# Performance work log

Hardware: AMD Instinct MI355X
Metric: run time of the kernel (lower is better)

Reference implementation:

```python
import jax, jax.numpy as jnp
import numpy as np

# Model / data dimensions
B, N, F_ATOM, V = 256, 256, 9, 128   # graphs, nodes/graph, atom feat cols, padded vocab
EMB, HID, DEPTH = 256, 32, 3          # emb_dim, hidden_channels=32 (fixed in source), depth
RATIO = 0.5                            # pool_ratios


def setup_inputs() -> dict:
    key = jax.random.key(0)
    ks = jax.random.split(key, 10)
    p = 16.0 / N  # avg degree ~16
    u = jax.random.uniform(ks[0], (B, N, N))
    adj = (u < p).astype(jnp.float32)
    adj = jnp.maximum(adj, adj.transpose(0, 2, 1))  # symmetric
    adj = adj * (1.0 - jnp.eye(N, dtype=jnp.float32))  # no self loops
    x_atom = jax.random.randint(ks[1], (B, N, F_ATOM), 0, 119)
    s = lambda k, sh, fan: jax.random.normal(k, sh) * (1.0 / np.sqrt(fan))
    return dict(
        adj=adj,
        x_atom=x_atom,
        atom_table=jax.random.normal(ks[2], (F_ATOM, V, EMB)) * 0.02,
        w_down0=s(ks[3], (EMB, HID), EMB), b_down0=jnp.zeros((HID,)),
        w_down=s(ks[4], (DEPTH, HID, HID), HID), b_down=jnp.zeros((DEPTH, HID)),
        w_pool=jax.random.normal(ks[5], (DEPTH, HID)),
        w_up=s(ks[6], (DEPTH - 1, HID, HID), HID), b_up=jnp.zeros((DEPTH - 1, HID)),
        w_up_last=s(ks[7], (HID, EMB), HID), b_up_last=jnp.zeros((EMB,)),
    )


def _gcn(x, A, W, b):
    # GCNConv(improved=True): Ahat = A + 2I, sym-normalized; A has zero diag.
    n = A.shape[-1]
    Ah = A + 2.0 * jnp.eye(n, dtype=A.dtype)
    d = jnp.sum(Ah, axis=-1)
    di = jnp.where(d > 0, jax.lax.rsqrt(jnp.maximum(d, 1e-12)), 0.0)
    An = Ah * di[:, :, None] * di[:, None, :]
    return jnp.einsum('bij,bjd->bid', An, x @ W) + b


def _augment(A):
    # remove self loops, add self loops (w=1), A @ A (spspmm), remove self loops
    n = A.shape[-1]
    eye = jnp.eye(n, dtype=A.dtype)
    A1 = A * (1.0 - eye) + eye
    A2 = jnp.einsum('bij,bjk->bik', A1, A1)
    return A2 * (1.0 - eye)


def _topk(x, A, w):
    # TopKPooling: score = tanh(x.w / ||w||); keep top ceil(ratio*n) per graph
    score = jnp.tanh((x @ w) / jnp.linalg.norm(w))  # [B, n]
    k = int(np.ceil(RATIO * x.shape[1]))
    vals, idx = jax.lax.top_k(score, k)  # [B, k]
    xg = jnp.take_along_axis(x, idx[:, :, None], axis=1) * vals[:, :, None]
    Ar = jnp.take_along_axis(A, idx[:, :, None], axis=1)
    Ag = jnp.take_along_axis(Ar, idx[:, None, :], axis=2)
    return xg, Ag, idx


def reference(adj, x_atom, atom_table, w_down0, b_down0, w_down, b_down,
              w_pool, w_up, b_up, w_up_last, b_up_last):
    # AtomEncoder: sum of per-column embeddings -> [B, N, EMB]
    h = jnp.sum(atom_table[jnp.arange(F_ATOM), x_atom], axis=2)

    # GraphUNet encode (sum_res=True, act=relu)
    x = jax.nn.relu(_gcn(h, adj, w_down0, b_down0))
    A = adj
    xs, As, perms = [x], [A], []
    for i in range(DEPTH):
        A = _augment(A)
        x, A, idx = _topk(x, A, w_pool[i])
        x = jax.nn.relu(_gcn(x, A, w_down[i], b_down[i]))
        if i < DEPTH - 1:
            xs.append(x)
            As.append(A)
        perms.append(idx)

    for i in range(DEPTH):
        j = DEPTH - 1 - i
        res, A, idx = xs[j], As[j], perms[j]
        b_idx = jnp.arange(B)[:, None]
        up = jnp.zeros_like(res).at[b_idx, idx].set(x)
        x = res + up
        if i < DEPTH - 1:
            x = jax.nn.relu(_gcn(x, A, w_up[i], b_up[i]))
        else:
            x = _gcn(x, A, w_up_last, b_up_last)

    # global_add_pool over nodes of each graph -> [B, EMB]
    return jnp.sum(x, axis=1)
```

## Files before the change

kernel.cpp:

```cpp
#include <hip/hip_runtime.h>
#include <stdint.h>
#include <math.h>

#define NB 256
#define NN 256
#define HC 32
#define EMBD 256
#define NF 9
#define NV 128
#define TPB 1024

typedef unsigned int u32;
typedef unsigned long long u64;

__global__ void k_tw(const float* __restrict__ table, const float* __restrict__ W0,
                     float* __restrict__ TW) {
    int gid = blockIdx.x * 256 + threadIdx.x;
    if (gid >= NF * NV * HC) return;
    int c = gid & 31;
    int v = (gid >> 5) & (NV - 1);
    int f = gid >> 12;
    const float* trow = table + (size_t)(f * NV + v) * EMBD;
    float acc = 0.f;
    for (int e = 0; e < EMBD; ++e) acc += trow[e] * W0[e * HC + c];
    TW[gid] = acc;
}

#define SM_BITS   0
#define SM_DI0    8192
#define SM_BIG0   9216
#define SM_X1     46080
#define SM_BIG1   64512
#define SM_X2     82944
#define SM_BIG2   92160
#define SM_ZB     101376
#define SM_WG     119808
#define SM_SC     124416
#define SM_KEYS   125440
#define SM_IDX0   127488
#define SM_VALS0  128000
#define SM_INV0   128512
#define SM_IDX1   129536
#define SM_VALS1  129792
#define SM_INV1   130048
#define SM_IDX2   130560
#define SM_VALS2  130688
#define SM_INV2   130816
#define SM_DI1    131072
#define SM_DI2    131584
#define SM_DI3    131840
#define SM_PART   131968
#define SM_GL     136192
#define SM_TOTAL  136320

__device__ __forceinline__ u32 dot4acc(u32 a, u32 b, u32 c) {
#if __has_builtin(__builtin_amdgcn_udot4)
    return __builtin_amdgcn_udot4(a, b, c, false);
#else
    return c + (a & 0xffu) * (b & 0xffu) + ((a >> 8) & 0xffu) * ((b >> 8) & 0xffu)
         + ((a >> 16) & 0xffu) * ((b >> 16) & 0xffu) + (a >> 24) * (b >> 24);
#endif
}

template <int N, int K>
__device__ __forceinline__ void topk_rank(const float* sc, u64* keys,
                                          int* idxo, float* valso, int* invo, int t) {
    if (t < N) {
        invo[t] = -1;
        float s = sc[t];
        u32 bits = __float_as_uint(s);
        u32 m = ((int)bits < 0) ? 0xFFFFFFFFu : 0x80000000u;
        u32 ordv = ~(bits ^ m);
        keys[t] = ((u64)ordv << 32) | (u32)t;
    }
    __syncthreads();
    if (t < N) {
        u64 mykey = keys[t];
        int rank = 0;
#pragma unroll 8
        for (int j = 0; j < N; ++j) rank += (keys[j] < mykey) ? 1 : 0;
        if (rank < K) {
            idxo[rank] = t;
            valso[rank] = sc[t];
            invo[t] = rank;
        }
    }
    __syncthreads();
}

template <int N>
__device__ __forceinline__ void az_f32(const float* A, const float* z,
                                       const float* di, const float* __restrict__ bias,
                                       float* xout, int t) {
    if (t < N * 8) {
        int r = t >> 3, cq = (t & 7) * 4;
        float a0 = 0.f, a1 = 0.f, a2 = 0.f, a3 = 0.f;
        for (int jj = 0; jj < N; ++jj) {
            const float4 zv = *reinterpret_cast<const float4*>(&z[jj * 36 + cq]);
            float a = A[jj * N + r];
            a0 += a * zv.x; a1 += a * zv.y; a2 += a * zv.z; a3 += a * zv.w;
        }
        float dr = di[r];
        float4 o;
        o.x = fmaxf(dr * (a0 + 2.f * z[r * 36 + cq + 0]) + bias[cq + 0], 0.f);
        o.y = fmaxf(dr * (a1 + 2.f * z[r * 36 + cq + 1]) + bias[cq + 1], 0.f);
        o.z = fmaxf(dr * (a2 + 2.f * z[r * 36 + cq + 2]) + bias[cq + 2], 0.f);
        o.w = fmaxf(dr * (a3 + 2.f * z[r * 36 + cq + 3]) + bias[cq + 3], 0.f);
        *reinterpret_cast<float4*>(&xout[r * 36 + cq]) = o;
    }
    __syncthreads();
}

__device__ __forceinline__ void az_u8(const u32* AgW, const float* z,
                                      const float* di, const float* __restrict__ bias,
                                      float* xout, int t) {
    int r = t >> 3, cq = (t & 7) * 4;
    int wsel = r >> 2, bsh = (r & 3) * 8;
    float a0 = 0.f, a1 = 0.f, a2 = 0.f, a3 = 0.f;
    for (int jj = 0; jj < 128; ++jj) {
        const float4 zv = *reinterpret_cast<const float4*>(&z[jj * 36 + cq]);
        float f = (float)((AgW[jj * 32 + wsel] >> bsh) & 255u);
        a0 += f * zv.x; a1 += f * zv.y; a2 += f * zv.z; a3 += f * zv.w;
    }
    float dr = di[r];
    float4 o;
    o.x = fmaxf(dr * (a0 + 2.f * z[r * 36 + cq + 0]) + bias[cq + 0], 0.f);
    o.y = fmaxf(dr * (a1 + 2.f * z[r * 36 + cq + 1]) + bias[cq + 1], 0.f);
    o.z = fmaxf(dr * (a2 + 2.f * z[r * 36 + cq + 2]) + bias[cq + 2], 0.f);
    o.w = fmaxf(dr * (a3 + 2.f * z[r * 36 + cq + 3]) + bias[cq + 3], 0.f);
    *reinterpret_cast<float4*>(&xout[r * 36 + cq]) = o;
    __syncthreads();
}

template <int N>
__device__ __forceinline__ void xw_mm(const float* xin, const float* Wl,
                                      const float* pre, float* zout, int t) {
    for (int i = t; i < N * 8; i += TPB) {
        int r = i >> 3, cq = (i & 7) * 4;
        float a0 = 0.f, a1 = 0.f, a2 = 0.f, a3 = 0.f;
#pragma unroll 8
        for (int e = 0; e < 32; ++e) {
            float xv = xin[r * 36 + e];
            const float4 wv = *reinterpret_cast<const float4*>(&Wl[e * 36 + cq]);
            a0 += xv * wv.x; a1 += xv * wv.y; a2 += xv * wv.z; a3 += xv * wv.w;
        }
        float p = pre ? pre[r] : 1.f;
        *reinterpret_cast<float4*>(&zout[r * 36 + cq]) =
            make_float4(a0 * p, a1 * p, a2 * p, a3 * p);
    }
    __syncthreads();
}

template <int N>
__device__ __forceinline__ void deg_lds(const float* A, float* di, int t) {
    if (t < N) {
        float acc = 0.f;
        for (int i = 0; i < N; ++i) acc += A[i * N + t];
        di[t] = 1.0f / sqrtf(acc + 2.0f);
    }
    __syncthreads();
}

__device__ __forceinline__ void deg_u8(const u32* AgW, float* di, int t) {
    if (t < 128) {
        u32 acc = 0;
        for (int w = 0; w < 32; ++w)
            acc = dot4acc(AgW[t * 32 + ((w + t) & 31)], 0x01010101u, acc);
        di[t] = 1.0f / sqrtf((float)acc + 2.0f);
    }
    __syncthreads();
}

__device__ __forceinline__ void aug64_32(const float* A, const int* idxl,
                                         float* out, int t) {
    if (t < 256) {
        int rr0 = t >> 3, sb = (t & 7) * 4;
        int ir = idxl[rr0];
        int is0 = idxl[sb], is1 = idxl[sb + 1], is2 = idxl[sb + 2], is3 = idxl[sb + 3];
        float c0 = 0.f, c1 = 0.f, c2 = 0.f, c3 = 0.f;
        for (int jj = 0; jj < 16; ++jj) {
            int jq = ((jj + rr0) & 15) * 4;
            const float4 ar = *reinterpret_cast<const float4*>(&A[ir * 64 + jq]);
            const float4 v0 = *reinterpret_cast<const float4*>(&A[is0 * 64 + jq]);
            const float4 v1 = *reinterpret_cast<const float4*>(&A[is1 * 64 + jq]);
            const float4 v2 = *reinterpret_cast<const float4*>(&A[is2 * 64 + jq]);
            const float4 v3 = *reinterpret_cast<const float4*>(&A[is3 * 64 + jq]);
            c0 += ar.x * v0.x + ar.y * v0.y + ar.z * v0.z + ar.w * v0.w;
            c1 += ar.x * v1.x + ar.y * v1.y + ar.z * v1.z + ar.w * v1.w;
            c2 += ar.x * v2.x + ar.y * v2.y + ar.z * v2.z + ar.w * v2.w;
            c3 += ar.x * v3.x + ar.y * v3.y + ar.z * v3.z + ar.w * v3.w;
        }
        float o0 = c0 + 2.f * A[ir * 64 + is0] + (ir == is0 ? 1.f : 0.f);
        float o1 = c1 + 2.f * A[ir * 64 + is1] + (ir == is1 ? 1.f : 0.f);
        float o2 = c2 + 2.f * A[ir * 64 + is2] + (ir == is2 ? 1.f : 0.f);
        float o3 = c3 + 2.f * A[ir * 64 + is3] + (ir == is3 ? 1.f : 0.f);
        if (rr0 == sb + 0) o0 = 0.f;
        if (rr0 == sb + 1) o1 = 0.f;
        if (rr0 == sb + 2) o2 = 0.f;
        if (rr0 == sb + 3) o3 = 0.f;
        *reinterpret_cast<float4*>(&out[rr0 * 32 + sb]) = make_float4(o0, o1, o2, o3);
    }
    __syncthreads();
}

__global__ void __launch_bounds__(TPB, 1) k_mega(
    const float* __restrict__ adj, const float* __restrict__ TW,
    const int* __restrict__ xa,
    const float* __restrict__ bd0, const float* __restrict__ wd,
    const float* __restrict__ bd, const float* __restrict__ wp,
    const float* __restrict__ wu, const float* __restrict__ bu,
    const float* __restrict__ wul, const float* __restrict__ bul,
    float* __restrict__ gx0, float* __restrict__ outp) {
    __shared__ __align__(16) char SM[SM_TOTAL];
    u32*   bitsl = (u32*)(SM + SM_BITS);
    float* di0l  = (float*)(SM + SM_DI0);
    float* z0    = (float*)(SM + SM_BIG0);
    u32*   AgW   = (u32*)(SM + SM_BIG0);
    float* x1l   = (float*)(SM + SM_X1);
    float* big1  = (float*)(SM + SM_BIG1);
    float* x2l   = (float*)(SM + SM_X2);
    float* big2  = (float*)(SM + SM_BIG2);
    float* zbf   = (float*)(SM + SM_ZB);
    u32*   Pg    = (u32*)(SM + SM_WG);
    float* Wl    = (float*)(SM + SM_WG);
    float* scl   = (float*)(SM + SM_SC);
    u64*   keys  = (u64*)(SM + SM_KEYS);
    int*   idx0l = (int*)(SM + SM_IDX0);
    float* vals0l= (float*)(SM + SM_VALS0);
    int*   inv0l = (int*)(SM + SM_INV0);
    int*   idx1l = (int*)(SM + SM_IDX1);
    float* vals1l= (float*)(SM + SM_VALS1);
    int*   inv1l = (int*)(SM + SM_INV1);
    int*   idx2l = (int*)(SM + SM_IDX2);
    float* vals2l= (float*)(SM + SM_VALS2);
    int*   inv2l = (int*)(SM + SM_INV2);
    float* di1   = (float*)(SM + SM_DI1);
    float* di2   = (float*)(SM + SM_DI2);
    float* di3   = (float*)(SM + SM_DI3);
    float* part  = (float*)(SM + SM_PART);
    float* gl    = (float*)(SM + SM_GL);
    float* x3l   = big2 + 1024;
    float* dec64 = big2;
    float* dec128= big1;

    int b = blockIdx.x, t = threadIdx.x;

    for (int i = t; i < 2048; i += TPB) {
        int node = i >> 3, cq = (i & 7) * 4;
        const int* xr = xa + (b * NN + node) * NF;
        float ax = 0.f, ay = 0.f, azz = 0.f, aw = 0.f;
#pragma unroll
        for (int f = 0; f < NF; ++f) {
            int v = xr[f];
            const float4 tw = *reinterpret_cast<const float4*>(&TW[((f << 7) + v) * HC + cq]);
            ax += tw.x; ay += tw.y; azz += tw.z; aw += tw.w;
        }
        *reinterpret_cast<float4*>(&z0[node * 36 + cq]) = make_float4(ax, ay, azz, aw);
    }

    {
        int lane = t & 63, wv = t >> 6;
        for (int row = wv; row < NN; row += 16) {
            const float* ar = adj + ((size_t)b * NN + row) * NN;
            int deg = 0;
#pragma unroll
            for (int p = 0; p < 4; ++p) {
                u64 m = __ballot(ar[p * 64 + lane] != 0.0f);
                if (lane == 0) {
                    bitsl[row * 8 + 2 * p]     = (u32)m;
                    bitsl[row * 8 + 2 * p + 1] = (u32)(m >> 32);
                    deg += __popcll(m);
                }
            }
            if (lane == 0) di0l[row] = 1.0f / sqrtf((float)deg + 2.0f);
        }
    }
    if (t < 32) gl[t] = wp[t];
    __syncthreads();

    {
        float sn0 = 0.f;
        for (int i = 0; i < HC; ++i) { float v = gl[i]; sn0 += v * v; }
        sn0 = sqrtf(sn0);
        int r0 = t >> 3, cq = (t & 7) * 4;
        for (int tile = 0; tile < 2; ++tile) {
            int r = tile * 128 + r0;
            u32 mw[8];
#pragma unroll
            for (int w = 0; w < 8; ++w) mw[w] = bitsl[r * 8 + w];
            float a0 = 0.f, a1 = 0.f, a2 = 0.f, a3 = 0.f;
#pragma unroll
            for (int w = 0; w < 8; ++w) {
                u32 m = mw[w];
                int base = w * 32;
                while (m) {
                    int j = base + __ffs(m) - 1;
                    m &= m - 1;
                    float dj = di0l[j];
                    const float4 zv = *reinterpret_cast<const float4*>(&z0[j * 36 + cq]);
                    a0 += dj * zv.x; a1 += dj * zv.y; a2 += dj * zv.z; a3 += dj * zv.w;
                }
            }
            float dr = di0l[r];
            float o0 = fmaxf(dr * (a0 + 2.f * dr * z0[r * 36 + cq + 0]) + bd0[cq + 0], 0.f);
            float o1 = fmaxf(dr * (a1 + 2.f * dr * z0[r * 36 + cq + 1]) + bd0[cq + 1], 0.f);
            float o2 = fmaxf(dr * (a2 + 2.f * dr * z0[r * 36 + cq + 2]) + bd0[cq + 2], 0.f);
            float o3 = fmaxf(dr * (a3 + 2.f * dr * z0[r * 36 + cq + 3]) + bd0[cq + 3], 0.f);
            *reinterpret_cast<float4*>(&gx0[((size_t)b * NN + r) * HC + cq]) =
                make_float4(o0, o1, o2, o3);
            float pd = o0 * gl[cq] + o1 * gl[cq + 1] + o2 * gl[cq + 2] + o3 * gl[cq + 3];
            pd += __shfl_xor(pd, 1);
            pd += __shfl_xor(pd, 2);
            pd += __shfl_xor(pd, 4);
            if ((t & 7) == 0) scl[r] = tanhf(pd / sn0);
        }
    }
    __syncthreads();

    topk_rank<256, 128>(scl, keys, idx0l, vals0l, inv0l, t);

    if (t < 1024) {
        int r = t >> 3, w = t & 7;
        int row = idx0l[r];
        u32 word = bitsl[row * 8 + w];
        if (w == (row >> 5)) word |= (1u << (row & 31));
        Pg[r * 9 + w] = word;
    }
    __syncthreads();
    {
        int rr0 = t >> 4, sb = (t & 15) * 4;
        u32 rw[2][8];
#pragma unroll
        for (int rt = 0; rt < 2; ++rt)
#pragma unroll
            for (int w = 0; w < 8; ++w) rw[rt][w] = Pg[(rt * 64 + rr0) * 9 + w];
#pragma unroll
        for (int k4 = 0; k4 < 2; ++k4) {
            int s0 = sb + 64 * k4;
            u32 cnt[2][4];
#pragma unroll
            for (int a = 0; a < 2; ++a) { cnt[a][0] = cnt[a][1] = cnt[a][2] = cnt[a][3] = 0; }
#pragma unroll
            for (int u = 0; u < 4; ++u) {
                int s = s0 + u;
#pragma unroll
                for (int w = 0; w < 8; ++w) {
                    u32 sw = Pg[s * 9 + w];
                    cnt[0][u] += __popc(rw[0][w] & sw);
                    cnt[1][u] += __popc(rw[1][w] & sw);
                }
            }
#pragma unroll
            for (int rt = 0; rt < 2; ++rt) {
                int r = rt * 64 + rr0;
                if (r >= s0 && r < s0 + 4) cnt[rt][r - s0] = 0;
                AgW[r * 32 + (s0 >> 2)] =
                    cnt[rt][0] | (cnt[rt][1] << 8) | (cnt[rt][2] << 16) | (cnt[rt][3] << 24);
            }
        }
    }
    __syncthreads();

    deg_u8(AgW, di1, t);

    if (t < 1024) Wl[(t >> 5) * 36 + (t & 31)] = wd[t];
    {
        int r = t >> 3, cq = (t & 7) * 4;
        float s = di1[r] * vals0l[r];
        const float4 xv = *reinterpret_cast<const float4*>(
            &gx0[((size_t)b * NN + idx0l[r]) * HC + cq]);
        *reinterpret_cast<float4*>(&big1[r * 36 + cq]) =
            make_float4(s * xv.x, s * xv.y, s * xv.z, s * xv.w);
    }
    __syncthreads();
    xw_mm<128>(big1, Wl, nullptr, zbf, t);
    az_u8(AgW, zbf, di1, bd, x1l, t);

    if (t < 32) gl[t] = wp[32 + t];
    __syncthreads();
    {
        float sn = 0.f;
        for (int i = 0; i < HC; ++i) { float v = gl[i]; sn += v * v; }
        sn = sqrtf(sn);
        if (t < 128) {
            float acc = 0.f;
#pragma unroll
            for (int i = 0; i < HC; ++i) {
                int c = (i + t) & 31;
                acc += x1l[t * 36 + c] * gl[c];
            }
            scl[t] = tanhf(acc / sn);
        }
    }
    __syncthreads();
    topk_rank<128, 64>(scl, keys, idx1l, vals1l, inv1l, t);

    {
        u32* Gb = (u32*)zbf;
        for (int i = t; i < 2048; i += TPB) {
            int k = i >> 5, w = i & 31;
            int ir = idx1l[k];
            u32 word = AgW[ir * 32 + w];
            if (w == (ir >> 2)) word += (1u << (8 * (ir & 3)));
            Gb[k * 33 + w] = word;
        }
        __syncthreads();
        {
            int r = t >> 4, sq = t & 15;
            u32 racc[4] = {0, 0, 0, 0};
            for (int w = 0; w < 32; ++w) {
                u32 rv = Gb[r * 33 + w];
                racc[0] = dot4acc(rv, Gb[(sq * 4 + 0) * 33 + w], racc[0]);
                racc[1] = dot4acc(rv, Gb[(sq * 4 + 1) * 33 + w], racc[1]);
                racc[2] = dot4acc(rv, Gb[(sq * 4 + 2) * 33 + w], racc[2]);
                racc[3] = dot4acc(rv, Gb[(sq * 4 + 3) * 33 + w], racc[3]);
            }
            float4 o;
            o.x = (r == sq * 4 + 0) ? 0.f : (float)racc[0];
            o.y = (r == sq * 4 + 1) ? 0.f : (float)racc[1];
            o.z = (r == sq * 4 + 2) ? 0.f : (float)racc[2];
            o.w = (r == sq * 4 + 3) ? 0.f : (float)racc[3];
            *reinterpret_cast<float4*>(&big1[r * 64 + sq * 4]) = o;
        }
        __syncthreads();
    }

    deg_lds<64>(big1, di2, t);

    if (t < 1024) Wl[(t >> 5) * 36 + (t & 31)] = wd[1024 + t];
    if (t < 512) {
        float* xg1 = zbf + 2304;
        int r = t >> 3, cq = (t & 7) * 4;
        float s = di2[r] * vals1l[r];
        const float4 xv = *reinterpret_cast<const float4*>(&x1l[idx1l[r] * 36 + cq]);
        *reinterpret_cast<float4*>(&xg1[r * 36 + cq]) =
            make_float4(s * xv.x, s * xv.y, s * xv.z, s * xv.w);
    }
    __syncthreads();
    xw_mm<64>(zbf + 2304, Wl, nullptr, zbf, t);
    az_f32<64>(big1, zbf, di2, bd + 32, x2l, t);

    if (t < 32) gl[t] = wp[64 + t];
    __syncthreads();
    {
        float sn = 0.f;
        for (int i = 0; i < HC; ++i) { float v = gl[i]; sn += v * v; }
        sn = sqrtf(sn);
        if (t < 64) {
            float acc = 0.f;
#pragma unroll
            for (int i = 0; i < HC; ++i) {
                int c = (i + t) & 31;
                acc += x2l[t * 36 + c] * gl[c];
            }
            scl[t] = tanhf(acc / sn);
        }
    }
    __syncthreads();
    topk_rank<64, 32>(scl, keys, idx2l, vals2l, inv2l, t);

    aug64_32(big1, idx2l, big2, t);

    deg_lds<32>(big2, di3, t);

    if (t < 1024) Wl[(t >> 5) * 36 + (t & 31)] = wd[2048 + t];
    if (t < 256) {
        float* xg2 = zbf + 2304;
        int r = t >> 3, cq = (t & 7) * 4;
        float s = di3[r] * vals2l[r];
        const float4 xv = *reinterpret_cast<const float4*>(&x2l[idx2l[r] * 36 + cq]);
        *reinterpret_cast<float4*>(&xg2[r * 36 + cq]) =
            make_float4(s * xv.x, s * xv.y, s * xv.z, s * xv.w);
    }
    __syncthreads();
    xw_mm<32>(zbf + 2304, Wl, nullptr, zbf, t);
    az_f32<32>(big2, zbf, di3, bd + 64, x3l, t);

    if (t < 2048) {
        int r = t >> 5, c = t & 31;
        if (t < 2048 && r < 64) {
            int ir = inv2l[r];
            if (ir >= 0) x2l[r * 36 + c] += x3l[ir * 36 + c];
        }
    }
    if (t < 1024) Wl[(t >> 5) * 36 + (t & 31)] = wu[t];
    __syncthreads();
    xw_mm<64>(x2l, Wl, di2, zbf, t);
    az_f32<64>(big1, zbf, di2, bu, dec64, t);

    for (int i = t; i < 4096; i += TPB) {
        int r = i >> 5, c = i & 31;
        int ir = inv1l[r];
        if (ir >= 0) x1l[r * 36 + c] += dec64[ir * 36 + c];
    }
    if (t < 1024) Wl[(t >> 5) * 36 + (t & 31)] = wu[1024 + t];
    __syncthreads();
    xw_mm<128>(x1l, Wl, di1, zbf, t);
    az_u8(AgW, zbf, di1, bu + 32, dec128, t);

    if (t < 256) {
        float acc = 0.f;
        u32 mw[8];
#pragma unroll
        for (int w = 0; w < 8; ++w) mw[w] = bitsl[t * 8 + w];
#pragma unroll
        for (int w = 0; w < 8; ++w) {
            u32 m = mw[w];
            int base = w * 32;
            while (m) {
                int i = base + __ffs(m) - 1;
                m &= m - 1;
                acc += di0l[i];
            }
        }
        scl[t] = di0l[t] * (acc + 2.f * di0l[t]);
    }
    __syncthreads();
    {
        int c = t & 31, jg = t >> 5;
        float a2 = 0.f;
        for (int j = jg * 8; j < jg * 8 + 8; ++j) {
            int ir = inv0l[j];
            float xv = gx0[((size_t)b * NN + j) * HC + c];
            if (ir >= 0) xv += dec128[ir * 36 + c];
            a2 += scl[j] * xv;
        }
        part[jg * 33 + c] = a2;
    }
    __syncthreads();
    if (t < 32) {
        float g = 0.f;
#pragma unroll
        for (int q = 0; q < 32; ++q) g += part[q * 33 + t];
        gl[t] = g;
    }
    __syncthreads();
    if (t < 256) {
        float a3 = 0.f;
        for (int cc = 0; cc < HC; ++cc) a3 += gl[cc] * wul[cc * EMBD + t];
        outp[b * EMBD + t] = a3 + 256.0f * bul[t];
    }
}

extern "C" void kernel_launch(void* const* d_in, const int* in_sizes, int n_in,
                              void* d_out, int out_size, void* d_ws, size_t ws_size,
                              hipStream_t stream) {
    const float* adj       = (const float*)d_in[0];
    const int*   xatom     = (const int*)d_in[1];
    const float* table     = (const float*)d_in[2];
    const float* w_down0   = (const float*)d_in[3];
    const float* b_down0   = (const float*)d_in[4];
    const float* w_down    = (const float*)d_in[5];
    const float* b_down    = (const float*)d_in[6];
    const float* w_pool    = (const float*)d_in[7];
    const float* w_up      = (const float*)d_in[8];
    const float* b_up      = (const float*)d_in[9];
    const float* w_up_last = (const float*)d_in[10];
    const float* b_up_last = (const float*)d_in[11];
    float* outp = (float*)d_out;

    float* ws = (float*)d_ws;
    float* TW  = ws;
    float* gx0 = ws + 36928;

    k_tw<<<(NF * NV * HC + 255) / 256, 256, 0, stream>>>(table, w_down0, TW);
    k_mega<<<NB, TPB, 0, stream>>>(adj, TW, xatom,
                                   b_down0, w_down, b_down, w_pool,
                                   w_up, b_up, w_up_last, b_up_last,
                                   gx0, outp);
}
```

Before: 99.79 us.

## Fuse degree computation, topk key build, and residual merges to cut barriers

New measurement: 100.2 us. No clear change (+0.4%).

```diff
diff --git a/kernel.cpp b/kernel.cpp
--- a/kernel.cpp
+++ b/kernel.cpp
@@ -62,18 +62,22 @@
 #endif
 }
 
+__device__ __forceinline__ float ftanh(float x) {
+    float ax = fabsf(x);
+    float e = __expf(-2.f * ax);
+    float tv = (1.f - e) / (1.f + e);
+    return copysignf(tv, x);
+}
+
+__device__ __forceinline__ u64 mkkey(float s, int r) {
+    u32 bits = __float_as_uint(s);
+    u32 m = ((int)bits < 0) ? 0xFFFFFFFFu : 0x80000000u;
+    return ((u64)(~(bits ^ m)) << 32) | (u32)r;
+}
+
 template <int N, int K>
-__device__ __forceinline__ void topk_rank(const float* sc, u64* keys,
+__device__ __forceinline__ void rank_pass(const float* sc, const u64* keys,
                                           int* idxo, float* valso, int* invo, int t) {
-    if (t < N) {
-        invo[t] = -1;
-        float s = sc[t];
-        u32 bits = __float_as_uint(s);
-        u32 m = ((int)bits < 0) ? 0xFFFFFFFFu : 0x80000000u;
-        u32 ordv = ~(bits ^ m);
-        keys[t] = ((u64)ordv << 32) | (u32)t;
-    }
-    __syncthreads();
     if (t < N) {
         u64 mykey = keys[t];
         int rank = 0;
@@ -152,27 +156,30 @@
 }
 
 template <int N>
-__device__ __forceinline__ void deg_lds(const float* A, float* di, int t) {
-    if (t < N) {
-        float acc = 0.f;
-        for (int i = 0; i < N; ++i) acc += A[i * N + t];
-        di[t] = 1.0f / sqrtf(acc + 2.0f);
-    }
-    __syncthreads();
-}
-
-__device__ __forceinline__ void deg_u8(const u32* AgW, float* di, int t) {
-    if (t < 128) {
-        u32 acc = 0;
-        for (int w = 0; w < 32; ++w)
-            acc = dot4acc(AgW[t * 32 + ((w + t) & 31)], 0x01010101u, acc);
-        di[t] = 1.0f / sqrtf((float)acc + 2.0f);
+__device__ __forceinline__ void xw_mrg(const float* xin, const float* xup,
+                                       const int* invl, const float* Wl,
+                                       const float* pre, float* zout, int t) {
+    for (int i = t; i < N * 8; i += TPB) {
+        int r = i >> 3, cq = (i & 7) * 4;
+        int ir = invl[r];
+        const float* ux = (ir >= 0) ? &xup[ir * 36] : nullptr;
+        float a0 = 0.f, a1 = 0.f, a2 = 0.f, a3 = 0.f;
+#pragma unroll 8
+        for (int e = 0; e < 32; ++e) {
+            float xv = xin[r * 36 + e];
+            if (ux) xv += ux[e];
+            const float4 wv = *reinterpret_cast<const float4*>(&Wl[e * 36 + cq]);
+            a0 += xv * wv.x; a1 += xv * wv.y; a2 += xv * wv.z; a3 += xv * wv.w;
+        }
+        float p = pre[r];
+        *reinterpret_cast<float4*>(&zout[r * 36 + cq]) =
+            make_float4(a0 * p, a1 * p, a2 * p, a3 * p);
     }
     __syncthreads();
 }
 
 __device__ __forceinline__ void aug64_32(const float* A, const int* idxl,
-                                         float* out, int t) {
+                                         float* out, float* di3, int t) {
     if (t < 256) {
         int rr0 = t >> 3, sb = (t & 7) * 4;
         int ir = idxl[rr0];
@@ -199,6 +206,11 @@
         if (rr0 == sb + 2) o2 = 0.f;
         if (rr0 == sb + 3) o3 = 0.f;
         *reinterpret_cast<float4*>(&out[rr0 * 32 + sb]) = make_float4(o0, o1, o2, o3);
+        float ps = o0 + o1 + o2 + o3;
+        ps += __shfl_xor(ps, 1);
+        ps += __shfl_xor(ps, 2);
+        ps += __shfl_xor(ps, 4);
+        if ((t & 7) == 0) di3[rr0] = 1.0f / sqrtf(ps + 2.0f);
     }
     __syncthreads();
 }
@@ -312,14 +324,19 @@
             pd += __shfl_xor(pd, 1);
             pd += __shfl_xor(pd, 2);
             pd += __shfl_xor(pd, 4);
-            if ((t & 7) == 0) scl[r] = tanhf(pd / sn0);
-        }
-    }
-    __syncthreads();
-
-    topk_rank<256, 128>(scl, keys, idx0l, vals0l, inv0l, t);
-
-    if (t < 1024) {
+            if ((t & 7) == 0) {
+                float s = ftanh(pd / sn0);
+                scl[r] = s;
+                keys[r] = mkkey(s, r);
+                inv0l[r] = -1;
+            }
+        }
+    }
+    __syncthreads();
+
+    rank_pass<256, 128>(scl, keys, idx0l, vals0l, inv0l, t);
+
+    {
         int r = t >> 3, w = t & 7;
         int row = idx0l[r];
         u32 word = bitsl[row * 8 + w];
@@ -334,6 +351,7 @@
         for (int rt = 0; rt < 2; ++rt)
 #pragma unroll
             for (int w = 0; w < 8; ++w) rw[rt][w] = Pg[(rt * 64 + rr0) * 9 + w];
+        int rs0 = 0, rs1 = 0;
 #pragma unroll
         for (int k4 = 0; k4 < 2; ++k4) {
             int s0 = sb + 64 * k4;
@@ -356,14 +374,23 @@
                 if (r >= s0 && r < s0 + 4) cnt[rt][r - s0] = 0;
                 AgW[r * 32 + (s0 >> 2)] =
                     cnt[rt][0] | (cnt[rt][1] << 8) | (cnt[rt][2] << 16) | (cnt[rt][3] << 24);
-            }
-        }
-    }
-    __syncthreads();
-
-    deg_u8(AgW, di1, t);
+                int sum4 = (int)(cnt[rt][0] + cnt[rt][1] + cnt[rt][2] + cnt[rt][3]);
+                if (rt == 0) rs0 += sum4; else rs1 += sum4;
+            }
+        }
+        rs0 += __shfl_xor(rs0, 1); rs0 += __shfl_xor(rs0, 2);
+        rs0 += __shfl_xor(rs0, 4); rs0 += __shfl_xor(rs0, 8);
+        rs1 += __shfl_xor(rs1, 1); rs1 += __shfl_xor(rs1, 2);
+        rs1 += __shfl_xor(rs1, 4); rs1 += __shfl_xor(rs1, 8);
+        if ((t & 15) == 0) {
+            di1[rr0]      = 1.0f / sqrtf((float)rs0 + 2.0f);
+            di1[rr0 + 64] = 1.0f / sqrtf((float)rs1 + 2.0f);
+        }
+    }
+    __syncthreads();
 
     if (t < 1024) Wl[(t >> 5) * 36 + (t & 31)] = wd[t];
+    if (t < 32) gl[t] = wp[32 + t];
     {
         int r = t >> 3, cq = (t & 7) * 4;
         float s = di1[r] * vals0l[r];
@@ -374,10 +401,9 @@
     }
     __syncthreads();
     xw_mm<128>(big1, Wl, nullptr, zbf, t);
+    if (t < 1024) Wl[(t >> 5) * 36 + (t & 31)] = wd[1024 + t];
     az_u8(AgW, zbf, di1, bd, x1l, t);
 
-    if (t < 32) gl[t] = wp[32 + t];
-    __syncthreads();
     {
         float sn = 0.f;
         for (int i = 0; i < HC; ++i) { float v = gl[i]; sn += v * v; }
@@ -389,11 +415,14 @@
                 int c = (i + t) & 31;
                 acc += x1l[t * 36 + c] * gl[c];
             }
-            scl[t] = tanhf(acc / sn);
-        }
-    }
-    __syncthreads();
-    topk_rank<128, 64>(scl, keys, idx1l, vals1l, inv1l, t);
+            float s = ftanh(acc / sn);
+            scl[t] = s;
+            keys[t] = mkkey(s, t);
+            inv1l[t] = -1;
+        }
+    }
+    __syncthreads();
+    rank_pass<128, 64>(scl, keys, idx1l, vals1l, inv1l, t);
 
     {
         u32* Gb = (u32*)zbf;
@@ -421,13 +450,15 @@
             o.z = (r == sq * 4 + 2) ? 0.f : (float)racc[2];
             o.w = (r == sq * 4 + 3) ? 0.f : (float)racc[3];
             *reinterpret_cast<float4*>(&big1[r * 64 + sq * 4]) = o;
+            float ps = o.x + o.y + o.z + o.w;
+            ps += __shfl_xor(ps, 1); ps += __shfl_xor(ps, 2);
+            ps += __shfl_xor(ps, 4); ps += __shfl_xor(ps, 8);
+            if (sq == 0) di2[r] = 1.0f / sqrtf(ps + 2.0f);
         }
         __syncthreads();
     }
 
-    deg_lds<64>(big1, di2, t);
-
-    if (t < 1024) Wl[(t >> 5) * 36 + (t & 31)] = wd[1024 + t];
+    if (t < 32) gl[t] = wp[64 + t];
     if (t < 512) {
         float* xg1 = zbf + 2304;
         int r = t >> 3, cq = (t & 7) * 4;
@@ -438,10 +469,9 @@
     }
     __syncthreads();
     xw_mm<64>(zbf + 2304, Wl, nullptr, zbf, t);
+    if (t < 1024) Wl[(t >> 5) * 36 + (t & 31)] = wd[2048 + t];
     az_f32<64>(big1, zbf, di2, bd + 32, x2l, t);
 
-    if (t < 32) gl[t] = wp[64 + t];
-    __syncthreads();
     {
         float sn = 0.f;
         for (int i = 0; i < HC; ++i) { float v = gl[i]; sn += v * v; }
@@ -453,17 +483,17 @@
                 int c = (i + t) & 31;
                 acc += x2l[t * 36 + c] * gl[c];
             }
-            scl[t] = tanhf(acc / sn);
-        }
-    }
-    __syncthreads();
-    topk_rank<64, 32>(scl, keys, idx2l, vals2l, inv2l, t);
-
-    aug64_32(big1, idx2l, big2, t);
-
-    deg_lds<32>(big2, di3, t);
-
-    if (t < 1024) Wl[(t >> 5) * 36 + (t & 31)] = wd[2048 + t];
+            float s = ftanh(acc / sn);
+            scl[t] = s;
+            keys[t] = mkkey(s, t);
+            inv2l[t] = -1;
+        }
+    }
+    __syncthreads();
+    rank_pass<64, 32>(scl, keys, idx2l, vals2l, inv2l, t);
+
+    aug64_32(big1, idx2l, big2, di3, t);
+
     if (t < 256) {
         float* xg2 = zbf + 2304;
         int r = t >> 3, cq = (t & 7) * 4;
@@ -474,57 +504,48 @@
     }
     __syncthreads();
     xw_mm<32>(zbf + 2304, Wl, nullptr, zbf, t);
+    if (t < 1024) Wl[(t >> 5) * 36 + (t & 31)] = wu[t];
     az_f32<32>(big2, zbf, di3, bd + 64, x3l, t);
 
-    if (t < 2048) {
-        int r = t >> 5, c = t & 31;
-        if (t < 2048 && r < 64) {
-            int ir = inv2l[r];
-            if (ir >= 0) x2l[r * 36 + c] += x3l[ir * 36 + c];
-        }
-    }
-    if (t < 1024) Wl[(t >> 5) * 36 + (t & 31)] = wu[t];
-    __syncthreads();
-    xw_mm<64>(x2l, Wl, di2, zbf, t);
+    xw_mrg<64>(x2l, x3l, inv2l, Wl, di2, zbf, t);
+    if (t < 1024) Wl[(t >> 5) * 36 + (t & 31)] = wu[1024 + t];
     az_f32<64>(big1, zbf, di2, bu, dec64, t);
 
-    for (int i = t; i < 4096; i += TPB) {
-        int r = i >> 5, c = i & 31;
-        int ir = inv1l[r];
-        if (ir >= 0) x1l[r * 36 + c] += dec64[ir * 36 + c];
-    }
-    if (t < 1024) Wl[(t >> 5) * 36 + (t & 31)] = wu[1024 + t];
-    __syncthreads();
-    xw_mm<128>(x1l, Wl, di1, zbf, t);
+    xw_mrg<128>(x1l, dec64, inv1l, Wl, di1, zbf, t);
     az_u8(AgW, zbf, di1, bu + 32, dec128, t);
 
-    if (t < 256) {
-        float acc = 0.f;
-        u32 mw[8];
-#pragma unroll
-        for (int w = 0; w < 8; ++w) mw[w] = bitsl[t * 8 + w];
-#pragma unroll
-        for (int w = 0; w < 8; ++w) {
-            u32 m = mw[w];
-            int base = w * 32;
-            while (m) {
-                int i = base + __ffs(m) - 1;
-                m &= m - 1;
-                acc += di0l[i];
-            }
-        }
-        scl[t] = di0l[t] * (acc + 2.f * di0l[t]);
-    }
-    __syncthreads();
     {
         int c = t & 31, jg = t >> 5;
+        float xv[8];
+#pragma unroll
+        for (int k = 0; k < 8; ++k) {
+            int j = jg * 8 + k;
+            float v = gx0[((size_t)b * NN + j) * HC + c];
+            int ir = inv0l[j];
+            if (ir >= 0) v += dec128[ir * 36 + c];
+            xv[k] = v;
+        }
+        if (t < 256) {
+            float acc = 0.f;
+            u32 mw[8];
+#pragma unroll
+            for (int w = 0; w < 8; ++w) mw[w] = bitsl[t * 8 + w];
+#pragma unroll
+            for (int w = 0; w < 8; ++w) {
+                u32 m = mw[w];
+                int base = w * 32;
+                while (m) {
+                    int i = base + __ffs(m) - 1;
+                    m &= m - 1;
+                    acc += di0l[i];
+                }
+            }
+            scl[t] = di0l[t] * (acc + 2.f * di0l[t]);
+        }
+        __syncthreads();
         float a2 = 0.f;
-        for (int j = jg * 8; j < jg * 8 + 8; ++j) {
-            int ir = inv0l[j];
-            float xv = gx0[((size_t)b * NN + j) * HC + c];
-            if (ir >= 0) xv += dec128[ir * 36 + c];
-            a2 += scl[j] * xv;
-        }
+#pragma unroll
+        for (int k = 0; k < 8; ++k) a2 += scl[jg * 8 + k] * xv[k];
         part[jg * 33 + c] = a2;
     }
     __syncthreads();
```
